# Performance work log

Hardware: AMD Instinct MI355X
Metric: run time of the kernel (lower is better)

The kernel has to match this reference:

```python
import jax, jax.numpy as jnp
import numpy as np

N_USER = 50_000
N_ITEM = 100_000
N = N_USER + N_ITEM          # total graph nodes
E = 2_400_000                # nnz of normalized adjacency (avg degree ~16)
D = 64                       # emb_size; layers = [64, 64, 64]
SLOPE = 0.2                  # NGCF uses LeakyReLU(alpha=0.2)


def setup_inputs() -> dict:
    key = jax.random.key(0)
    ks = jax.random.split(key, 20)
    inp = {
        "user_emb": jax.random.normal(ks[0], (N_USER, D), jnp.float32) * 0.1,
        "item_emb": jax.random.normal(ks[1], (N_ITEM, D), jnp.float32) * 0.1,
    }
    for k in range(3):
        inp[f"W_gc_{k}"] = jax.random.normal(ks[2 + 4 * k], (D, D), jnp.float32) * 0.1
        inp[f"b_gc_{k}"] = jax.random.normal(ks[3 + 4 * k], (1, D), jnp.float32) * 0.1
        inp[f"W_bi_{k}"] = jax.random.normal(ks[4 + 4 * k], (D, D), jnp.float32) * 0.1
        inp[f"b_bi_{k}"] = jax.random.normal(ks[5 + 4 * k], (1, D), jnp.float32) * 0.1
    inp["adj_vals"] = jax.random.uniform(ks[14], (E,), jnp.float32) * (1.0 / 16.0)
    inp["adj_rows"] = jax.random.randint(ks[15], (E,), 0, N, jnp.int32)
    inp["adj_cols"] = jax.random.randint(ks[16], (E,), 0, N, jnp.int32)
    return inp


def _l2norm(x):
    n = jnp.linalg.norm(x, axis=1, keepdims=True)
    return x / jnp.maximum(n, 1e-12)


def reference(user_emb, item_emb,
              W_gc_0, b_gc_0, W_bi_0, b_bi_0,
              W_gc_1, b_gc_1, W_bi_1, b_bi_1,
              W_gc_2, b_gc_2, W_bi_2, b_bi_2,
              adj_vals, adj_rows, adj_cols):
    Wg = [W_gc_0, W_gc_1, W_gc_2]
    bg = [b_gc_0, b_gc_1, b_gc_2]
    Wb = [W_bi_0, W_bi_1, W_bi_2]
    bb = [b_bi_0, b_bi_1, b_bi_2]

    ego = jnp.concatenate([user_emb, item_emb], axis=0)  # [N, D]
    all_embs = [ego]
    for k in range(3):
        # side = norm_adj @ ego  (sparse COO spmm via gather + segment_sum)
        msgs = adj_vals[:, None] * ego[adj_cols]          # [E, D]
        side = jax.ops.segment_sum(msgs, adj_rows, num_segments=N)
        sum_emb = jax.nn.leaky_relu(side @ Wg[k] + bg[k], SLOPE)
        bi_emb = jax.nn.leaky_relu((ego * side) @ Wb[k] + bb[k], SLOPE)
        ego = sum_emb + bi_emb
        all_embs.append(_l2norm(ego))
    return jnp.concatenate(all_embs, axis=1)              # [N, 4*D]
```

## Files before the change

kernel.cpp:

```cpp
#include <hip/hip_runtime.h>

#define N_TOT      150000
#define N_USER     50000
#define N_EDGE     2400000
#define DIM        64
#define OUT_STRIDE 256
#define SLOPE      0.2f
#define NB_SCAN    ((N_TOT + 255) / 256)


__global__ void init_ego(const float* __restrict__ ue, const float* __restrict__ ie,
                         float* __restrict__ ego, float* __restrict__ out) {
    int idx = blockIdx.x * blockDim.x + threadIdx.x;
    if (idx >= N_TOT * DIM / 4) return;
    int n  = idx >> 4;
    int c4 = idx & 15;
    float4 v = (n < N_USER) ? ((const float4*)ue)[idx]
                            : ((const float4*)ie)[idx - N_USER * (DIM / 4)];
    ((float4*)ego)[idx] = v;
    ((float4*)out)[n * (OUT_STRIDE / 4) + c4] = v;
}

__global__ void hist_rank(const int* __restrict__ rows, int* __restrict__ cnt,
                          int* __restrict__ rank) {
    int t = blockIdx.x * blockDim.x + threadIdx.x;
    if (t >= N_EDGE / 4) return;
    int4 r4 = ((const int4*)rows)[t];
    int4 k4;
    k4.x = atomicAdd(&cnt[r4.x], 1);
    k4.y = atomicAdd(&cnt[r4.y], 1);
    k4.z = atomicAdd(&cnt[r4.z], 1);
    k4.w = atomicAdd(&cnt[r4.w], 1);
    ((int4*)rank)[t] = k4;
}

__global__ __launch_bounds__(256) void scan_partial(const int* __restrict__ cnt,
                                                    int* __restrict__ row_ptr,
                                                    int* __restrict__ bsum) {
    __shared__ int s[256];
    int tid = threadIdx.x;
    int i = blockIdx.x * 256 + tid;
    int v = (i < N_TOT) ? cnt[i] : 0;
    s[tid] = v;
    __syncthreads();
    for (int off = 1; off < 256; off <<= 1) {
        int t = (tid >= off) ? s[tid - off] : 0;
        __syncthreads();
        s[tid] += t;
        __syncthreads();
    }
    if (i < N_TOT) row_ptr[i] = s[tid] - v;
    if (tid == 255) bsum[blockIdx.x] = s[255];
}

__global__ __launch_bounds__(1024) void scan_bsums(int* __restrict__ bsum) {
    __shared__ int s[1024];
    int tid = threadIdx.x;
    int v = (tid < NB_SCAN) ? bsum[tid] : 0;
    s[tid] = v;
    __syncthreads();
    for (int off = 1; off < 1024; off <<= 1) {
        int t = (tid >= off) ? s[tid - off] : 0;
        __syncthreads();
        s[tid] += t;
        __syncthreads();
    }
    if (tid < NB_SCAN) bsum[tid] = s[tid] - v;
}

__global__ __launch_bounds__(256) void add_offsets(int* __restrict__ row_ptr,
                                                   const int* __restrict__ bsum) {
    int i = blockIdx.x * 256 + threadIdx.x;
    if (i < N_TOT) row_ptr[i] += bsum[blockIdx.x];
    if (i == 0) row_ptr[N_TOT] = N_EDGE;
}

__global__ void scatter_edges(const int* __restrict__ rows, const int* __restrict__ cols,
                              const float* __restrict__ vals,
                              const int* __restrict__ row_ptr,
                              const int* __restrict__ rank, int2* __restrict__ epack) {
    int t = blockIdx.x * blockDim.x + threadIdx.x;
    if (t >= N_EDGE / 4) return;
    int4   r4 = ((const int4*)rows)[t];
    int4   k4 = ((const int4*)rank)[t];
    int4   c4 = ((const int4*)cols)[t];
    float4 v4 = ((const float4*)vals)[t];
    epack[row_ptr[r4.x] + k4.x] = make_int2(c4.x, __float_as_int(v4.x));
    epack[row_ptr[r4.y] + k4.y] = make_int2(c4.y, __float_as_int(v4.y));
    epack[row_ptr[r4.z] + k4.z] = make_int2(c4.z, __float_as_int(v4.z));
    epack[row_ptr[r4.w] + k4.w] = make_int2(c4.w, __float_as_int(v4.w));
}

__global__ __launch_bounds__(256) void spmm_gather(
    const int* __restrict__ row_ptr, const int2* __restrict__ epack,
    const float* __restrict__ ego, float* __restrict__ side) {
    int lane = threadIdx.x & 63;
    int row  = blockIdx.x * 4 + (threadIdx.x >> 6);
    if (row >= N_TOT) return;
    int beg = row_ptr[row];
    int end = row_ptr[row + 1];
    int g = lane >> 4;
    int q = lane & 15;
    float4 acc = make_float4(0.f, 0.f, 0.f, 0.f);
    int i = beg;
    for (; i + 8 <= end; i += 8) {
        int4 ee = ((const int4*)(epack + i))[g];
        float4 va = ((const float4*)(ego + (size_t)ee.x * DIM))[q];
        float4 vb = ((const float4*)(ego + (size_t)ee.z * DIM))[q];
        float wa = __int_as_float(ee.y);
        float wb = __int_as_float(ee.w);
        acc.x = fmaf(wa, va.x, acc.x); acc.y = fmaf(wa, va.y, acc.y);
        acc.z = fmaf(wa, va.z, acc.z); acc.w = fmaf(wa, va.w, acc.w);
        acc.x = fmaf(wb, vb.x, acc.x); acc.y = fmaf(wb, vb.y, acc.y);
        acc.z = fmaf(wb, vb.z, acc.z); acc.w = fmaf(wb, vb.w, acc.w);
    }
    for (; i < end; i += 4) {
        if (i + g < end) {
            int2 e = epack[i + g];
            float4 v = ((const float4*)(ego + (size_t)e.x * DIM))[q];
            float w = __int_as_float(e.y);
            acc.x = fmaf(w, v.x, acc.x); acc.y = fmaf(w, v.y, acc.y);
            acc.z = fmaf(w, v.z, acc.z); acc.w = fmaf(w, v.w, acc.w);
        }
    }
    acc.x += __shfl_xor(acc.x, 16, 64); acc.y += __shfl_xor(acc.y, 16, 64);
    acc.z += __shfl_xor(acc.z, 16, 64); acc.w += __shfl_xor(acc.w, 16, 64);
    acc.x += __shfl_xor(acc.x, 32, 64); acc.y += __shfl_xor(acc.y, 32, 64);
    acc.z += __shfl_xor(acc.z, 32, 64); acc.w += __shfl_xor(acc.w, 32, 64);
    if (g == 0)
        *(float4*)(side + (size_t)row * DIM + q * 4) = acc;
}

__global__ __launch_bounds__(256) void transform_gemm(
    const float* __restrict__ Wg, const float* __restrict__ bgv,
    const float* __restrict__ Wb, const float* __restrict__ bbv,
    const float* __restrict__ side, float* __restrict__ ego,
    float* __restrict__ out, int layer) {
    __shared__ float sST[DIM][68];
    __shared__ float sPT[DIM][68];
    __shared__ float sWg[DIM][DIM];
    __shared__ float sWb[DIM][DIM];
    int tid = threadIdx.x;
    int R0  = blockIdx.x * 64;

    #pragma unroll
    for (int it = 0; it < 4; ++it) {
        int f = tid + it * 256;
        float4 wg = ((const float4*)Wg)[f];
        float4 wb = ((const float4*)Wb)[f];
        int k = f >> 4, c = (f & 15) * 4;
        *(float4*)&sWg[k][c] = wg;
        *(float4*)&sWb[k][c] = wb;
    }
    #pragma unroll
    for (int it = 0; it < 4; ++it) {
        int f  = tid + it * 256;
        int r  = f >> 4, k0 = (f & 15) * 4;
        int row = R0 + r;
        float4 s4 = make_float4(0.f, 0.f, 0.f, 0.f);
        float4 e4 = make_float4(0.f, 0.f, 0.f, 0.f);
        if (row < N_TOT) {
            s4 = *(const float4*)&side[(size_t)row * DIM + k0];
            e4 = *(const float4*)&ego [(size_t)row * DIM + k0];
        }
        sST[k0 + 0][r] = s4.x; sST[k0 + 1][r] = s4.y;
        sST[k0 + 2][r] = s4.z; sST[k0 + 3][r] = s4.w;
        sPT[k0 + 0][r] = s4.x * e4.x; sPT[k0 + 1][r] = s4.y * e4.y;
        sPT[k0 + 2][r] = s4.z * e4.z; sPT[k0 + 3][r] = s4.w * e4.w;
    }
    __syncthreads();

    int tx = tid & 15, ty = tid >> 4;
    int c0 = tx * 4, r0 = ty * 4;
    float ag[4][4] = {{0.f}}, ab[4][4] = {{0.f}};
    #pragma unroll 4
    for (int k = 0; k < DIM; ++k) {
        float4 s4 = *(const float4*)&sST[k][r0];
        float4 p4 = *(const float4*)&sPT[k][r0];
        float4 g4 = *(const float4*)&sWg[k][c0];
        float4 b4 = *(const float4*)&sWb[k][c0];
        float ss[4] = {s4.x, s4.y, s4.z, s4.w};
        float pp[4] = {p4.x, p4.y, p4.z, p4.w};
        float gg[4] = {g4.x, g4.y, g4.z, g4.w};
        float bw[4] = {b4.x, b4.y, b4.z, b4.w};
        #pragma unroll
        for (int i = 0; i < 4; ++i)
            #pragma unroll
            for (int j = 0; j < 4; ++j) {
                ag[i][j] = fmaf(ss[i], gg[j], ag[i][j]);
                ab[i][j] = fmaf(pp[i], bw[j], ab[i][j]);
            }
    }

    float4 bg4 = *(const float4*)&bgv[c0];
    float4 bb4 = *(const float4*)&bbv[c0];
    float bgl[4] = {bg4.x, bg4.y, bg4.z, bg4.w};
    float bbl[4] = {bb4.x, bb4.y, bb4.z, bb4.w};

    float ne[4][4];
    float ss2[4];
    #pragma unroll
    for (int i = 0; i < 4; ++i) {
        float s = 0.f;
        #pragma unroll
        for (int j = 0; j < 4; ++j) {
            float g = ag[i][j] + bgl[j];
            float b = ab[i][j] + bbl[j];
            g = g > 0.f ? g : SLOPE * g;
            b = b > 0.f ? b : SLOPE * b;
            float v = g + b;
            ne[i][j] = v;
            s = fmaf(v, v, s);
        }
        ss2[i] = s;
    }
    #pragma unroll
    for (int m = 1; m < 16; m <<= 1) {
        #pragma unroll
        for (int i = 0; i < 4; ++i) ss2[i] += __shfl_xor(ss2[i], m, 64);
    }

    float* outbase = out + (size_t)(layer + 1) * DIM;
    #pragma unroll
    for (int i = 0; i < 4; ++i) {
        int row = R0 + r0 + i;
        if (row >= N_TOT) break;
        float inv = 1.f / fmaxf(sqrtf(ss2[i]), 1e-12f);
        float4 e4 = make_float4(ne[i][0], ne[i][1], ne[i][2], ne[i][3]);
        float4 o4 = make_float4(ne[i][0] * inv, ne[i][1] * inv, ne[i][2] * inv, ne[i][3] * inv);
        *(float4*)&ego[(size_t)row * DIM + c0] = e4;
        *(float4*)&outbase[(size_t)row * OUT_STRIDE + c0] = o4;
    }
}

extern "C" void kernel_launch(void* const* d_in, const int* in_sizes, int n_in,
                              void* d_out, int out_size, void* d_ws, size_t ws_size,
                              hipStream_t stream) {
    const float* ue = (const float*)d_in[0];
    const float* ie = (const float*)d_in[1];
    const float* Wg[3] = {(const float*)d_in[2], (const float*)d_in[6], (const float*)d_in[10]};
    const float* bg[3] = {(const float*)d_in[3], (const float*)d_in[7], (const float*)d_in[11]};
    const float* Wb[3] = {(const float*)d_in[4], (const float*)d_in[8], (const float*)d_in[12]};
    const float* bb[3] = {(const float*)d_in[5], (const float*)d_in[9], (const float*)d_in[13]};
    const float* vals = (const float*)d_in[14];
    const int*  rows  = (const int*)d_in[15];
    const int*  cols  = (const int*)d_in[16];
    float* out = (float*)d_out;

    float* ego     = (float*)d_ws;
    float* side    = ego + (size_t)N_TOT * DIM;
    int2*  epack   = (int2*)(side + (size_t)N_TOT * DIM);
    int*   row_ptr = (int*)(epack + N_EDGE);
    int*   cnt     = row_ptr + (N_TOT + 16);
    int*   bsum    = cnt + N_TOT;
    int*   rank    = (int*)side;

    hipMemsetAsync(cnt, 0, (size_t)N_TOT * sizeof(int), stream);
    hist_rank<<<(N_EDGE / 4 + 255) / 256, 256, 0, stream>>>(rows, cnt, rank);
    scan_partial<<<NB_SCAN, 256, 0, stream>>>(cnt, row_ptr, bsum);
    scan_bsums<<<1, 1024, 0, stream>>>(bsum);
    add_offsets<<<NB_SCAN, 256, 0, stream>>>(row_ptr, bsum);
    scatter_edges<<<(N_EDGE / 4 + 255) / 256, 256, 0, stream>>>(rows, cols, vals,
                                                                row_ptr, rank, epack);

    init_ego<<<(N_TOT * DIM / 4 + 255) / 256, 256, 0, stream>>>(ue, ie, ego, out);

    for (int k = 0; k < 3; ++k) {
        spmm_gather<<<(N_TOT + 3) / 4, 256, 0, stream>>>(row_ptr, epack, ego, side);
        transform_gemm<<<(N_TOT + 63) / 64, 256, 0, stream>>>(Wg[k], bg[k], Wb[k], bb[k],
                                                              side, ego, out, k);
    }
}
```

Before: 801.2 us.

## Fuse SpMM gather into transform GEMM and ping-pong ego buffers

Merges the per-layer SpMM gather and the dense transform into one kernel. Each block gathers its 64 rows' neighbour sums directly into shared memory and then runs the GEMM, so the side buffer is never written to or read back from global memory. Two ego buffers alternate between layers to avoid read/write hazards. The preprocessing kernels (hist_rank, scatter_edges) now handle 8 edges per thread. In exchange, blocks are far fewer (64 rows each instead of 4), and each block carries a large shared-memory footprint during the latency-bound gather. That may cut occupancy and latency hiding for the gather.

```diff
diff --git a/kernel.cpp b/kernel.cpp
--- a/kernel.cpp
+++ b/kernel.cpp
@@ -24,14 +24,20 @@
 __global__ void hist_rank(const int* __restrict__ rows, int* __restrict__ cnt,
                           int* __restrict__ rank) {
     int t = blockIdx.x * blockDim.x + threadIdx.x;
-    if (t >= N_EDGE / 4) return;
-    int4 r4 = ((const int4*)rows)[t];
-    int4 k4;
-    k4.x = atomicAdd(&cnt[r4.x], 1);
-    k4.y = atomicAdd(&cnt[r4.y], 1);
-    k4.z = atomicAdd(&cnt[r4.z], 1);
-    k4.w = atomicAdd(&cnt[r4.w], 1);
-    ((int4*)rank)[t] = k4;
+    if (t >= N_EDGE / 8) return;
+    int4 ra = ((const int4*)rows)[2 * t];
+    int4 rb = ((const int4*)rows)[2 * t + 1];
+    int4 ka, kb;
+    ka.x = atomicAdd(&cnt[ra.x], 1);
+    ka.y = atomicAdd(&cnt[ra.y], 1);
+    ka.z = atomicAdd(&cnt[ra.z], 1);
+    ka.w = atomicAdd(&cnt[ra.w], 1);
+    kb.x = atomicAdd(&cnt[rb.x], 1);
+    kb.y = atomicAdd(&cnt[rb.y], 1);
+    kb.z = atomicAdd(&cnt[rb.z], 1);
+    kb.w = atomicAdd(&cnt[rb.w], 1);
+    ((int4*)rank)[2 * t]     = ka;
+    ((int4*)rank)[2 * t + 1] = kb;
 }
 
 __global__ __launch_bounds__(256) void scan_partial(const int* __restrict__ cnt,
@@ -80,62 +86,27 @@
                               const int* __restrict__ row_ptr,
                               const int* __restrict__ rank, int2* __restrict__ epack) {
     int t = blockIdx.x * blockDim.x + threadIdx.x;
-    if (t >= N_EDGE / 4) return;
-    int4   r4 = ((const int4*)rows)[t];
-    int4   k4 = ((const int4*)rank)[t];
-    int4   c4 = ((const int4*)cols)[t];
-    float4 v4 = ((const float4*)vals)[t];
-    epack[row_ptr[r4.x] + k4.x] = make_int2(c4.x, __float_as_int(v4.x));
-    epack[row_ptr[r4.y] + k4.y] = make_int2(c4.y, __float_as_int(v4.y));
-    epack[row_ptr[r4.z] + k4.z] = make_int2(c4.z, __float_as_int(v4.z));
-    epack[row_ptr[r4.w] + k4.w] = make_int2(c4.w, __float_as_int(v4.w));
-}
-
-__global__ __launch_bounds__(256) void spmm_gather(
+    if (t >= N_EDGE / 8) return;
+    #pragma unroll
+    for (int h = 0; h < 2; ++h) {
+        int    f  = 2 * t + h;
+        int4   r4 = ((const int4*)rows)[f];
+        int4   k4 = ((const int4*)rank)[f];
+        int4   c4 = ((const int4*)cols)[f];
+        float4 v4 = ((const float4*)vals)[f];
+        epack[row_ptr[r4.x] + k4.x] = make_int2(c4.x, __float_as_int(v4.x));
+        epack[row_ptr[r4.y] + k4.y] = make_int2(c4.y, __float_as_int(v4.y));
+        epack[row_ptr[r4.z] + k4.z] = make_int2(c4.z, __float_as_int(v4.z));
+        epack[row_ptr[r4.w] + k4.w] = make_int2(c4.w, __float_as_int(v4.w));
+    }
+}
+
+__global__ __launch_bounds__(256) void fused_layer(
     const int* __restrict__ row_ptr, const int2* __restrict__ epack,
-    const float* __restrict__ ego, float* __restrict__ side) {
-    int lane = threadIdx.x & 63;
-    int row  = blockIdx.x * 4 + (threadIdx.x >> 6);
-    if (row >= N_TOT) return;
-    int beg = row_ptr[row];
-    int end = row_ptr[row + 1];
-    int g = lane >> 4;
-    int q = lane & 15;
-    float4 acc = make_float4(0.f, 0.f, 0.f, 0.f);
-    int i = beg;
-    for (; i + 8 <= end; i += 8) {
-        int4 ee = ((const int4*)(epack + i))[g];
-        float4 va = ((const float4*)(ego + (size_t)ee.x * DIM))[q];
-        float4 vb = ((const float4*)(ego + (size_t)ee.z * DIM))[q];
-        float wa = __int_as_float(ee.y);
-        float wb = __int_as_float(ee.w);
-        acc.x = fmaf(wa, va.x, acc.x); acc.y = fmaf(wa, va.y, acc.y);
-        acc.z = fmaf(wa, va.z, acc.z); acc.w = fmaf(wa, va.w, acc.w);
-        acc.x = fmaf(wb, vb.x, acc.x); acc.y = fmaf(wb, vb.y, acc.y);
-        acc.z = fmaf(wb, vb.z, acc.z); acc.w = fmaf(wb, vb.w, acc.w);
-    }
-    for (; i < end; i += 4) {
-        if (i + g < end) {
-            int2 e = epack[i + g];
-            float4 v = ((const float4*)(ego + (size_t)e.x * DIM))[q];
-            float w = __int_as_float(e.y);
-            acc.x = fmaf(w, v.x, acc.x); acc.y = fmaf(w, v.y, acc.y);
-            acc.z = fmaf(w, v.z, acc.z); acc.w = fmaf(w, v.w, acc.w);
-        }
-    }
-    acc.x += __shfl_xor(acc.x, 16, 64); acc.y += __shfl_xor(acc.y, 16, 64);
-    acc.z += __shfl_xor(acc.z, 16, 64); acc.w += __shfl_xor(acc.w, 16, 64);
-    acc.x += __shfl_xor(acc.x, 32, 64); acc.y += __shfl_xor(acc.y, 32, 64);
-    acc.z += __shfl_xor(acc.z, 32, 64); acc.w += __shfl_xor(acc.w, 32, 64);
-    if (g == 0)
-        *(float4*)(side + (size_t)row * DIM + q * 4) = acc;
-}
-
-__global__ __launch_bounds__(256) void transform_gemm(
+    const float* __restrict__ ego_in,
     const float* __restrict__ Wg, const float* __restrict__ bgv,
     const float* __restrict__ Wb, const float* __restrict__ bbv,
-    const float* __restrict__ side, float* __restrict__ ego,
-    float* __restrict__ out, int layer) {
+    float* __restrict__ ego_out, float* __restrict__ out, int layer) {
     __shared__ float sST[DIM][68];
     __shared__ float sPT[DIM][68];
     __shared__ float sWg[DIM][DIM];
@@ -152,21 +123,53 @@
         *(float4*)&sWg[k][c] = wg;
         *(float4*)&sWb[k][c] = wb;
     }
-    #pragma unroll
-    for (int it = 0; it < 4; ++it) {
-        int f  = tid + it * 256;
-        int r  = f >> 4, k0 = (f & 15) * 4;
-        int row = R0 + r;
-        float4 s4 = make_float4(0.f, 0.f, 0.f, 0.f);
-        float4 e4 = make_float4(0.f, 0.f, 0.f, 0.f);
+
+    int wave = tid >> 6;
+    int lane = tid & 63;
+    int g = lane >> 4;
+    int q = lane & 15;
+    for (int rr = wave; rr < 64; rr += 4) {
+        int row = R0 + rr;
+        float4 acc = make_float4(0.f, 0.f, 0.f, 0.f);
         if (row < N_TOT) {
-            s4 = *(const float4*)&side[(size_t)row * DIM + k0];
-            e4 = *(const float4*)&ego [(size_t)row * DIM + k0];
+            int beg = row_ptr[row];
+            int end = row_ptr[row + 1];
+            int i = beg;
+            for (; i + 8 <= end; i += 8) {
+                int4 ee = ((const int4*)(epack + i))[g];
+                float4 va = ((const float4*)(ego_in + (size_t)ee.x * DIM))[q];
+                float4 vb = ((const float4*)(ego_in + (size_t)ee.z * DIM))[q];
+                float wa = __int_as_float(ee.y);
+                float wb = __int_as_float(ee.w);
+                acc.x = fmaf(wa, va.x, acc.x); acc.y = fmaf(wa, va.y, acc.y);
+                acc.z = fmaf(wa, va.z, acc.z); acc.w = fmaf(wa, va.w, acc.w);
+                acc.x = fmaf(wb, vb.x, acc.x); acc.y = fmaf(wb, vb.y, acc.y);
+                acc.z = fmaf(wb, vb.z, acc.z); acc.w = fmaf(wb, vb.w, acc.w);
+            }
+            for (; i < end; i += 4) {
+                if (i + g < end) {
+                    int2 e = epack[i + g];
+                    float4 v = ((const float4*)(ego_in + (size_t)e.x * DIM))[q];
+                    float w = __int_as_float(e.y);
+                    acc.x = fmaf(w, v.x, acc.x); acc.y = fmaf(w, v.y, acc.y);
+                    acc.z = fmaf(w, v.z, acc.z); acc.w = fmaf(w, v.w, acc.w);
+                }
+            }
         }
-        sST[k0 + 0][r] = s4.x; sST[k0 + 1][r] = s4.y;
-        sST[k0 + 2][r] = s4.z; sST[k0 + 3][r] = s4.w;
-        sPT[k0 + 0][r] = s4.x * e4.x; sPT[k0 + 1][r] = s4.y * e4.y;
-        sPT[k0 + 2][r] = s4.z * e4.z; sPT[k0 + 3][r] = s4.w * e4.w;
+        acc.x += __shfl_xor(acc.x, 16, 64); acc.y += __shfl_xor(acc.y, 16, 64);
+        acc.z += __shfl_xor(acc.z, 16, 64); acc.w += __shfl_xor(acc.w, 16, 64);
+        acc.x += __shfl_xor(acc.x, 32, 64); acc.y += __shfl_xor(acc.y, 32, 64);
+        acc.z += __shfl_xor(acc.z, 32, 64); acc.w += __shfl_xor(acc.w, 32, 64);
+        if (g == 0) {
+            float4 e4 = make_float4(0.f, 0.f, 0.f, 0.f);
+            if (row < N_TOT)
+                e4 = *(const float4*)&ego_in[(size_t)row * DIM + q * 4];
+            int k0 = q * 4;
+            sST[k0 + 0][rr] = acc.x; sST[k0 + 1][rr] = acc.y;
+            sST[k0 + 2][rr] = acc.z; sST[k0 + 3][rr] = acc.w;
+            sPT[k0 + 0][rr] = acc.x * e4.x; sPT[k0 + 1][rr] = acc.y * e4.y;
+            sPT[k0 + 2][rr] = acc.z * e4.z; sPT[k0 + 3][rr] = acc.w * e4.w;
+        }
     }
     __syncthreads();
 
@@ -204,11 +207,11 @@
         float s = 0.f;
         #pragma unroll
         for (int j = 0; j < 4; ++j) {
-            float g = ag[i][j] + bgl[j];
-            float b = ab[i][j] + bbl[j];
-            g = g > 0.f ? g : SLOPE * g;
-            b = b > 0.f ? b : SLOPE * b;
-            float v = g + b;
+            float g2 = ag[i][j] + bgl[j];
+            float b2 = ab[i][j] + bbl[j];
+            g2 = g2 > 0.f ? g2 : SLOPE * g2;
+            b2 = b2 > 0.f ? b2 : SLOPE * b2;
+            float v = g2 + b2;
             ne[i][j] = v;
             s = fmaf(v, v, s);
         }
@@ -228,7 +231,7 @@
         float inv = 1.f / fmaxf(sqrtf(ss2[i]), 1e-12f);
         float4 e4 = make_float4(ne[i][0], ne[i][1], ne[i][2], ne[i][3]);
         float4 o4 = make_float4(ne[i][0] * inv, ne[i][1] * inv, ne[i][2] * inv, ne[i][3] * inv);
-        *(float4*)&ego[(size_t)row * DIM + c0] = e4;
+        *(float4*)&ego_out[(size_t)row * DIM + c0] = e4;
         *(float4*)&outbase[(size_t)row * OUT_STRIDE + c0] = o4;
     }
 }
@@ -247,27 +250,30 @@
     const int*  cols  = (const int*)d_in[16];
     float* out = (float*)d_out;
 
-    float* ego     = (float*)d_ws;
-    float* side    = ego + (size_t)N_TOT * DIM;
-    int2*  epack   = (int2*)(side + (size_t)N_TOT * DIM);
+    float* egoA    = (float*)d_ws;
+    float* egoB    = egoA + (size_t)N_TOT * DIM;
+    int2*  epack   = (int2*)(egoB + (size_t)N_TOT * DIM);
     int*   row_ptr = (int*)(epack + N_EDGE);
     int*   cnt     = row_ptr + (N_TOT + 16);
     int*   bsum    = cnt + N_TOT;
-    int*   rank    = (int*)side;
+    int*   rank    = (int*)egoB;
 
     hipMemsetAsync(cnt, 0, (size_t)N_TOT * sizeof(int), stream);
-    hist_rank<<<(N_EDGE / 4 + 255) / 256, 256, 0, stream>>>(rows, cnt, rank);
+    hist_rank<<<(N_EDGE / 8 + 255) / 256, 256, 0, stream>>>(rows, cnt, rank);
     scan_partial<<<NB_SCAN, 256, 0, stream>>>(cnt, row_ptr, bsum);
     scan_bsums<<<1, 1024, 0, stream>>>(bsum);
     add_offsets<<<NB_SCAN, 256, 0, stream>>>(row_ptr, bsum);
-    scatter_edges<<<(N_EDGE / 4 + 255) / 256, 256, 0, stream>>>(rows, cols, vals,
+    scatter_edges<<<(N_EDGE / 8 + 255) / 256, 256, 0, stream>>>(rows, cols, vals,
                                                                 row_ptr, rank, epack);
 
-    init_ego<<<(N_TOT * DIM / 4 + 255) / 256, 256, 0, stream>>>(ue, ie, ego, out);
-
+    init_ego<<<(N_TOT * DIM / 4 + 255) / 256, 256, 0, stream>>>(ue, ie, egoA, out);
+
+    const float* ein = egoA;
+    float*       eout = egoB;
     for (int k = 0; k < 3; ++k) {
-        spmm_gather<<<(N_TOT + 3) / 4, 256, 0, stream>>>(row_ptr, epack, ego, side);
-        transform_gemm<<<(N_TOT + 63) / 64, 256, 0, stream>>>(Wg[k], bg[k], Wb[k], bb[k],
-                                                              side, ego, out, k);
-    }
-}
+        fused_layer<<<(N_TOT + 63) / 64, 256, 0, stream>>>(row_ptr, epack, ein,
+                                                           Wg[k], bg[k], Wb[k], bb[k],
+                                                           eout, out, k);
+        const float* t = ein; ein = eout; eout = (float*)t;
+    }
+}
```

Result: slower. 1.102 ms (+37.5%).
